# Performance work log

Hardware: AMD Instinct MI355X
Metric: run time of the kernel (lower is better)

Reference implementation:

```python
import jax, jax.numpy as jnp
import numpy as np

B, C, H, W = 32, 512, 32, 32
N_WORDS, WORD_DIM = 77, 256
HW2 = H * W


def setup_inputs() -> dict:
    key = jax.random.key(0)
    k1, k2, k3 = jax.random.split(key, 3)
    feat = jax.random.normal(k1, (B, C, H, W), dtype=jnp.float32)
    word_emb = jax.random.normal(k2, (B, N_WORDS, WORD_DIM), dtype=jnp.float32)
    # nn.Linear(word_dim, img_hw*img_hw): weight (out,in), bias (out,)
    W_fc = jax.random.normal(k3, (HW2, WORD_DIM), dtype=jnp.float32) * (1.0 / np.sqrt(WORD_DIM))
    b_fc = jnp.zeros((HW2,), dtype=jnp.float32)
    return {"feat": feat, "word_emb": word_emb, "W_fc": W_fc, "b_fc": b_fc}


def reference(feat, word_emb, W_fc, b_fc):
    b, c, h, w = feat.shape
    f = feat.reshape(b, c, h * w)                                   # (b, c, hw2)
    we = jnp.einsum('bnd,kd->bnk', word_emb, W_fc) + b_fc           # (b, n, hw2)
    we = jnp.swapaxes(we, 1, 2)                                     # (b, hw2, n)
    scores = jnp.einsum('bck,bkn->bcn', f, we)                      # (b, c, n)
    att = jax.nn.softmax(scores, axis=-1)                           # (b, c, n)
    att_feat = jnp.einsum('bcn,bkn->bck', att, we)                  # (b, c, hw2)
    return att_feat.reshape(b, c, h, w)
```

## Files before the change

### kernel.cpp

```cpp
#include <hip/hip_runtime.h>

#define B_    32
#define C_    512
#define HW2_  1024
#define NW    77
#define NP    80
#define NPT   96
#define WD    256

typedef unsigned int   uint32;
typedef unsigned short u16;
typedef __attribute__((ext_vector_type(8))) short bf16x8;
typedef __attribute__((ext_vector_type(4))) float f32x4;

#define MFMA(a, b, c) __builtin_amdgcn_mfma_f32_16x16x32_bf16(a, b, c, 0, 0, 0)

#define WE_ELN   ((size_t)B_ * 16 * NP * 8)
#define WET_ELN  ((size_t)B_ * HW2_ * 12)
#define W_ELN    ((size_t)HW2_ * 32)
#define E_ELN    ((size_t)B_ * NP * 32)

__device__ __forceinline__ void split1(float x, u16 &h, u16 &l) {
    uint32 u = __float_as_uint(x);
    h = (u16)(u >> 16);
    float r = x - __uint_as_float(u & 0xffff0000u);
    uint32 v = __float_as_uint(r);
    l = (u16)((v + 0x7fffu + ((v >> 16) & 1u)) >> 16);
}

__device__ __forceinline__ void split8(float4 a, float4 b, bf16x8 &h, bf16x8 &l) {
    float v[8] = {a.x, a.y, a.z, a.w, b.x, b.y, b.z, b.w};
    #pragma unroll
    for (int i = 0; i < 8; ++i) {
        u16 hh, ll; split1(v[i], hh, ll);
        h[i] = (short)hh; l[i] = (short)ll;
    }
}

__global__ __launch_bounds__(256) void split_pre(
    const float* __restrict__ W_fc, const float* __restrict__ word_emb,
    bf16x8* __restrict__ Wh, bf16x8* __restrict__ Wl,
    bf16x8* __restrict__ Eh, bf16x8* __restrict__ El)
{
    const int g = blockIdx.x * 256 + threadIdx.x;
    if (g < (int)W_ELN) {
        float4 x = *(const float4*)(W_fc + g * 8);
        float4 y = *(const float4*)(W_fc + g * 8 + 4);
        bf16x8 h, l; split8(x, y, h, l);
        Wh[g] = h; Wl[g] = l;
    } else {
        const int e = g - (int)W_ELN;
        const int b = e / 2560, r = e % 2560;
        const int n = r >> 5, gg = r & 31;
        bf16x8 h = (bf16x8)(short)0, l = h;
        if (n < NW) {
            const float* p = word_emb + ((size_t)(b * NW + n)) * WD + gg * 8;
            float4 x = *(const float4*)p, y = *(const float4*)(p + 4);
            split8(x, y, h, l);
        }
        Eh[e] = h; El[e] = l;
    }
}

__global__ __launch_bounds__(256) void we_gemm(
    const bf16x8* __restrict__ Wh, const bf16x8* __restrict__ Wl,
    const bf16x8* __restrict__ Eh, const bf16x8* __restrict__ El,
    const float* __restrict__ b_fc,
    bf16x8* __restrict__ we_hi, bf16x8* __restrict__ we_lo,
    bf16x8* __restrict__ weT_hi, bf16x8* __restrict__ weT_lo)
{
    __shared__ __align__(16) uint32 HL[NP][68];

    const int id = blockIdx.x;
    const int b  = (id & 7) + 8 * (id >> 7);
    const int q  = (id >> 3) & 15;
    const int kb = q * 64;
    const int t  = threadIdx.x;
    const int w  = t >> 6, lane = t & 63, lr = lane & 15, lg = lane >> 4;
    const int kout = kb + 16 * w + lr;

    f32x4 acc[5];
    #pragma unroll
    for (int m = 0; m < 5; ++m) acc[m] = (f32x4)0.0f;

    const bf16x8* wrh = Wh + kout * 32;
    const bf16x8* wrl = Wl + kout * 32;
    const bf16x8* ebh = Eh + (b * NP + lr) * 32;
    const bf16x8* ebl = El + (b * NP + lr) * 32;

    #pragma unroll
    for (int ks = 0; ks < 8; ++ks) {
        const int o = ks * 4 + lg;
        const bf16x8 bh = wrh[o], bl = wrl[o];
        #pragma unroll
        for (int m = 0; m < 5; ++m) {
            const bf16x8 ah = ebh[m * 512 + o];
            const bf16x8 al = ebl[m * 512 + o];
            acc[m] = MFMA(ah, bh, acc[m]);
            acc[m] = MFMA(ah, bl, acc[m]);
            acc[m] = MFMA(al, bh, acc[m]);
            acc[m] = MFMA(al, bl, acc[m]);
        }
    }

    const float bias = b_fc[kout];
    #pragma unroll
    for (int m = 0; m < 5; ++m)
        #pragma unroll
        for (int r = 0; r < 4; ++r) {
            u16 hh, ll; split1(acc[m][r] + bias, hh, ll);
            HL[16 * m + 4 * lg + r][16 * w + lr] = ((uint32)hh << 16) | ll;
        }
    __syncthreads();

    #pragma unroll
    for (int u0 = 0; u0 < 640; u0 += 256) {
        const int u = u0 + t;
        if (u < 640) {
            const int n = u >> 3, c8 = (u & 7) * 8;
            uint4 p0 = *(const uint4*)&HL[n][c8];
            uint4 p1 = *(const uint4*)&HL[n][c8 + 4];
            const uint32 pw[8] = {p0.x, p0.y, p0.z, p0.w, p1.x, p1.y, p1.z, p1.w};
            bf16x8 hv, lv;
            #pragma unroll
            for (int i = 0; i < 8; ++i) {
                hv[i] = (short)(pw[i] >> 16);
                lv[i] = (short)(pw[i] & 0xffffu);
            }
            const int o = ((b * 16 + q) * NP + n) * 8 + (u & 7);
            we_hi[o] = hv; we_lo[o] = lv;
        }
    }
    #pragma unroll
    for (int v0 = 0; v0 < 1536; v0 += 256) {
        const int v = v0 + t;
        const int sel = v >= 768;
        const int r2  = sel ? v - 768 : v;
        const int row = r2 / 12, g = r2 % 12;
        bf16x8 val;
        #pragma unroll
        for (int i = 0; i < 8; ++i) {
            const int n = g * 8 + i;
            const uint32 p = (n < NP) ? HL[n][row] : 0u;
            val[i] = (short)(sel ? (p & 0xffffu) : (p >> 16));
        }
        (sel ? weT_lo : weT_hi)[(b * HW2_ + kb + row) * 12 + g] = val;
    }
}

__global__ __launch_bounds__(256, 2) void attn_mfma(
    const float* __restrict__ feat,
    const bf16x8* __restrict__ we_hi, const bf16x8* __restrict__ we_lo,
    const bf16x8* __restrict__ weT_hi, const bf16x8* __restrict__ weT_lo,
    float* __restrict__ out)
{
    __shared__ __align__(16) float S[4][16][84];
    __shared__ __align__(16) u16   Ph[32][NPT];
    __shared__ __align__(16) u16   Pl[32][NPT];

    const int id  = blockIdx.x;
    const int b   = (id & 7) + 8 * (id >> 7);
    const int c0  = ((id >> 3) & 15) * 32;

    const int t    = threadIdx.x;
    const int h    = t >> 6;
    const int lane = t & 63, lr = lane & 15, lg = lane >> 4;

    f32x4 acc[2][5];
    #pragma unroll
    for (int s = 0; s < 2; ++s)
        #pragma unroll
        for (int m = 0; m < 5; ++m) acc[s][m] = (f32x4)0.0f;

    const float* frow0 = feat + (size_t)(b * C_ + c0 + lr) * HW2_;
    const float* frow1 = frow0 + 16 * HW2_;

    #pragma unroll
    for (int ks = 0; ks < 8; ++ks) {
        const int kk = h * 256 + ks * 32 + 8 * lg;
        bf16x8 fh0, fl0, fh1, fl1;
        {   float4 x = *(const float4*)(frow0 + kk);
            float4 y = *(const float4*)(frow0 + kk + 4);
            split8(x, y, fh0, fl0); }
        {   float4 x = *(const float4*)(frow1 + kk);
            float4 y = *(const float4*)(frow1 + kk + 4);
            split8(x, y, fh1, fl1); }
        const int qb  = (b * 16 + h * 4 + (ks >> 1)) * NP;
        const int sub = (ks & 1) * 4 + lg;
        #pragma unroll
        for (int m = 0; m < 5; ++m) {
            const int o = (qb + 16 * m + lr) * 8 + sub;
            const bf16x8 ah = we_hi[o];
            const bf16x8 al = we_lo[o];
            acc[0][m] = MFMA(ah, fh0, acc[0][m]);
            acc[0][m] = MFMA(ah, fl0, acc[0][m]);
            acc[0][m] = MFMA(al, fh0, acc[0][m]);
            acc[1][m] = MFMA(ah, fh1, acc[1][m]);
            acc[1][m] = MFMA(ah, fl1, acc[1][m]);
            acc[1][m] = MFMA(al, fh1, acc[1][m]);
        }
    }

    #pragma unroll
    for (int s = 0; s < 2; ++s) {
        #pragma unroll
        for (int m = 0; m < 5; ++m)
            #pragma unroll
            for (int r = 0; r < 4; ++r)
                S[h][lr][16 * m + 4 * lg + r] = acc[s][m][r];
        __syncthreads();
        {
            const int srow = 4 * h + (lane >> 4), scol = lane & 15;
            float v5[6];
            float mx = -3.0e38f;
            #pragma unroll
            for (int j = 0; j < 6; ++j) {
                const int n = scol + 16 * j;
                float sv = 0.f;
                if (j < 5) {
                    sv = S[0][srow][n] + S[1][srow][n] + S[2][srow][n] + S[3][srow][n];
                    if (n < NW) mx = fmaxf(mx, sv);
                }
                v5[j] = sv;
            }
            mx = fmaxf(mx, __shfl_xor(mx, 1));
            mx = fmaxf(mx, __shfl_xor(mx, 2));
            mx = fmaxf(mx, __shfl_xor(mx, 4));
            mx = fmaxf(mx, __shfl_xor(mx, 8));
            float sum = 0.f;
            #pragma unroll
            for (int j = 0; j < 6; ++j) {
                const int n = scol + 16 * j;
                const float e = (n < NW) ? __expf(v5[j] - mx) : 0.f;
                v5[j] = e; sum += e;
            }
            sum += __shfl_xor(sum, 1);
            sum += __shfl_xor(sum, 2);
            sum += __shfl_xor(sum, 4);
            sum += __shfl_xor(sum, 8);
            const float inv = 1.0f / sum;
            #pragma unroll
            for (int j = 0; j < 6; ++j) {
                const int n = scol + 16 * j;
                u16 ph, pl; split1(v5[j] * inv, ph, pl);
                Ph[16 * s + srow][n] = ph; Pl[16 * s + srow][n] = pl;
            }
        }
        __syncthreads();
    }

    bf16x8 pbh[2][3], pbl[2][3];
    #pragma unroll
    for (int s = 0; s < 2; ++s)
        #pragma unroll
        for (int ksn = 0; ksn < 3; ++ksn) {
            pbh[s][ksn] = *(const bf16x8*)&Ph[16 * s + lr][32 * ksn + 8 * lg];
            pbl[s][ksn] = *(const bf16x8*)&Pl[16 * s + lr][32 * ksn + 8 * lg];
        }
    const bf16x8* th = weT_hi + (size_t)b * HW2_ * 12;
    const bf16x8* tl = weT_lo + (size_t)b * HW2_ * 12;
    float* orow0 = out + (size_t)(b * C_ + c0 + lr) * HW2_;
    float* orow1 = orow0 + 16 * HW2_;

    #pragma unroll
    for (int tt = 0; tt < 16; ++tt) {
        const int row = h * 256 + tt * 16 + lr;
        bf16x8 wa[3], wb[3];
        #pragma unroll
        for (int ksn = 0; ksn < 3; ++ksn) {
            wa[ksn] = th[row * 12 + 4 * ksn + lg];
            wb[ksn] = tl[row * 12 + 4 * ksn + lg];
        }
        f32x4 o0 = (f32x4)0.0f, o1 = (f32x4)0.0f;
        #pragma unroll
        for (int ksn = 0; ksn < 3; ++ksn) {
            o0 = MFMA(wa[ksn], pbh[0][ksn], o0);
            o0 = MFMA(wa[ksn], pbl[0][ksn], o0);
            o0 = MFMA(wb[ksn], pbh[0][ksn], o0);
            o1 = MFMA(wa[ksn], pbh[1][ksn], o1);
            o1 = MFMA(wa[ksn], pbl[1][ksn], o1);
            o1 = MFMA(wb[ksn], pbh[1][ksn], o1);
        }
        const int col = h * 256 + tt * 16 + 4 * lg;
        *(float4*)(orow0 + col) = make_float4(o0[0], o0[1], o0[2], o0[3]);
        *(float4*)(orow1 + col) = make_float4(o1[0], o1[1], o1[2], o1[3]);
    }
}

extern "C" void kernel_launch(void* const* d_in, const int* in_sizes, int n_in,
                              void* d_out, int out_size, void* d_ws, size_t ws_size,
                              hipStream_t stream) {
    (void)in_sizes; (void)n_in; (void)out_size; (void)ws_size;
    const float* feat     = (const float*)d_in[0];
    const float* word_emb = (const float*)d_in[1];
    const float* W_fc     = (const float*)d_in[2];
    const float* b_fc     = (const float*)d_in[3];

    bf16x8* we_hi  = (bf16x8*)d_ws;
    bf16x8* we_lo  = we_hi  + WE_ELN;
    bf16x8* weT_hi = we_lo  + WE_ELN;
    bf16x8* weT_lo = weT_hi + WET_ELN;
    bf16x8* Wh     = weT_lo + WET_ELN;
    bf16x8* Wl     = Wh + W_ELN;
    bf16x8* Eh     = Wl + W_ELN;
    bf16x8* El     = Eh + E_ELN;

    split_pre<<<448, 256, 0, stream>>>(W_fc, word_emb, Wh, Wl, Eh, El);
    we_gemm<<<512, 256, 0, stream>>>(Wh, Wl, Eh, El, b_fc, we_hi, we_lo, weT_hi, weT_lo);
    attn_mfma<<<512, 256, 0, stream>>>(feat, we_hi, we_lo, weT_hi, weT_lo, (float*)d_out);
}
```

Baseline: 182.1 us.

## Fuse bf16 split prepass into we_gemm and prefetch feat loads in attention

Removes the split_pre kernel and has we_gemm read fp32 W_fc and word_emb directly, splitting them into hi/lo bf16 in registers. This drops one launch and a round trip of the split intermediates through global memory. The attention kernel now issues all feat loads up front, behind a sched_barrier, before converting and running the MFMAs, so load latency overlaps better. The cost is higher register pressure in both kernels, and word_emb is re-split redundantly by every block that reads it.

Result: no change. 184.3 us (+1.2%).

```diff
diff --git a/kernel.cpp b/kernel.cpp
--- a/kernel.cpp
+++ b/kernel.cpp
@@ -17,8 +17,6 @@
 
 #define WE_ELN   ((size_t)B_ * 16 * NP * 8)
 #define WET_ELN  ((size_t)B_ * HW2_ * 12)
-#define W_ELN    ((size_t)HW2_ * 32)
-#define E_ELN    ((size_t)B_ * NP * 32)
 
 __device__ __forceinline__ void split1(float x, u16 &h, u16 &l) {
     uint32 u = __float_as_uint(x);
@@ -37,34 +35,8 @@
     }
 }
 
-__global__ __launch_bounds__(256) void split_pre(
-    const float* __restrict__ W_fc, const float* __restrict__ word_emb,
-    bf16x8* __restrict__ Wh, bf16x8* __restrict__ Wl,
-    bf16x8* __restrict__ Eh, bf16x8* __restrict__ El)
-{
-    const int g = blockIdx.x * 256 + threadIdx.x;
-    if (g < (int)W_ELN) {
-        float4 x = *(const float4*)(W_fc + g * 8);
-        float4 y = *(const float4*)(W_fc + g * 8 + 4);
-        bf16x8 h, l; split8(x, y, h, l);
-        Wh[g] = h; Wl[g] = l;
-    } else {
-        const int e = g - (int)W_ELN;
-        const int b = e / 2560, r = e % 2560;
-        const int n = r >> 5, gg = r & 31;
-        bf16x8 h = (bf16x8)(short)0, l = h;
-        if (n < NW) {
-            const float* p = word_emb + ((size_t)(b * NW + n)) * WD + gg * 8;
-            float4 x = *(const float4*)p, y = *(const float4*)(p + 4);
-            split8(x, y, h, l);
-        }
-        Eh[e] = h; El[e] = l;
-    }
-}
-
-__global__ __launch_bounds__(256) void we_gemm(
-    const bf16x8* __restrict__ Wh, const bf16x8* __restrict__ Wl,
-    const bf16x8* __restrict__ Eh, const bf16x8* __restrict__ El,
+__global__ __launch_bounds__(256, 2) void we_gemm(
+    const float* __restrict__ word_emb, const float* __restrict__ W_fc,
     const float* __restrict__ b_fc,
     bf16x8* __restrict__ we_hi, bf16x8* __restrict__ we_lo,
     bf16x8* __restrict__ weT_hi, bf16x8* __restrict__ weT_lo)
@@ -79,27 +51,46 @@
     const int w  = t >> 6, lane = t & 63, lr = lane & 15, lg = lane >> 4;
     const int kout = kb + 16 * w + lr;
 
+    const float* wrow = W_fc + kout * WD;
+    float4 wx[8], wy[8];
+    #pragma unroll
+    for (int ks = 0; ks < 8; ++ks) {
+        const int dk = ks * 32 + 8 * lg;
+        wx[ks] = *(const float4*)(wrow + dk);
+        wy[ks] = *(const float4*)(wrow + dk + 4);
+    }
+    __builtin_amdgcn_sched_barrier(0);
+
+    bf16x8 bh[8], bl[8];
+    #pragma unroll
+    for (int ks = 0; ks < 8; ++ks) split8(wx[ks], wy[ks], bh[ks], bl[ks]);
+
     f32x4 acc[5];
     #pragma unroll
     for (int m = 0; m < 5; ++m) acc[m] = (f32x4)0.0f;
 
-    const bf16x8* wrh = Wh + kout * 32;
-    const bf16x8* wrl = Wl + kout * 32;
-    const bf16x8* ebh = Eh + (b * NP + lr) * 32;
-    const bf16x8* ebl = El + (b * NP + lr) * 32;
+    const float* emb = word_emb + b * NW * WD;
 
     #pragma unroll
     for (int ks = 0; ks < 8; ++ks) {
-        const int o = ks * 4 + lg;
-        const bf16x8 bh = wrh[o], bl = wrl[o];
+        const int dk = ks * 32 + 8 * lg;
+        bf16x8 ah[5], al[5];
         #pragma unroll
         for (int m = 0; m < 5; ++m) {
-            const bf16x8 ah = ebh[m * 512 + o];
-            const bf16x8 al = ebl[m * 512 + o];
-            acc[m] = MFMA(ah, bh, acc[m]);
-            acc[m] = MFMA(ah, bl, acc[m]);
-            acc[m] = MFMA(al, bh, acc[m]);
-            acc[m] = MFMA(al, bl, acc[m]);
+            const int n = 16 * m + lr;
+            float4 x = make_float4(0.f, 0.f, 0.f, 0.f), y = x;
+            if (n < NW) {
+                const float* p = emb + n * WD + dk;
+                x = *(const float4*)p; y = *(const float4*)(p + 4);
+            }
+            split8(x, y, ah[m], al[m]);
+        }
+        #pragma unroll
+        for (int m = 0; m < 5; ++m) {
+            acc[m] = MFMA(ah[m], bh[ks], acc[m]);
+            acc[m] = MFMA(ah[m], bl[ks], acc[m]);
+            acc[m] = MFMA(al[m], bh[ks], acc[m]);
+            acc[m] = MFMA(al[m], bl[ks], acc[m]);
         }
     }
 
@@ -166,25 +157,31 @@
     const int h    = t >> 6;
     const int lane = t & 63, lr = lane & 15, lg = lane >> 4;
 
-    f32x4 acc[2][5];
-    #pragma unroll
-    for (int s = 0; s < 2; ++s)
-        #pragma unroll
-        for (int m = 0; m < 5; ++m) acc[s][m] = (f32x4)0.0f;
-
     const float* frow0 = feat + (size_t)(b * C_ + c0 + lr) * HW2_;
     const float* frow1 = frow0 + 16 * HW2_;
 
+    float4 f0x[8], f0y[8], f1x[8], f1y[8];
     #pragma unroll
     for (int ks = 0; ks < 8; ++ks) {
         const int kk = h * 256 + ks * 32 + 8 * lg;
+        f0x[ks] = *(const float4*)(frow0 + kk);
+        f0y[ks] = *(const float4*)(frow0 + kk + 4);
+        f1x[ks] = *(const float4*)(frow1 + kk);
+        f1y[ks] = *(const float4*)(frow1 + kk + 4);
+    }
+    __builtin_amdgcn_sched_barrier(0);
+
+    f32x4 acc[2][5];
+    #pragma unroll
+    for (int s = 0; s < 2; ++s)
+        #pragma unroll
+        for (int m = 0; m < 5; ++m) acc[s][m] = (f32x4)0.0f;
+
+    #pragma unroll
+    for (int ks = 0; ks < 8; ++ks) {
         bf16x8 fh0, fl0, fh1, fl1;
-        {   float4 x = *(const float4*)(frow0 + kk);
-            float4 y = *(const float4*)(frow0 + kk + 4);
-            split8(x, y, fh0, fl0); }
-        {   float4 x = *(const float4*)(frow1 + kk);
-            float4 y = *(const float4*)(frow1 + kk + 4);
-            split8(x, y, fh1, fl1); }
+        split8(f0x[ks], f0y[ks], fh0, fl0);
+        split8(f1x[ks], f1y[ks], fh1, fl1);
         const int qb  = (b * 16 + h * 4 + (ks >> 1)) * NP;
         const int sub = (ks & 1) * 4 + lg;
         #pragma unroll
@@ -300,12 +297,7 @@
     bf16x8* we_lo  = we_hi  + WE_ELN;
     bf16x8* weT_hi = we_lo  + WE_ELN;
     bf16x8* weT_lo = weT_hi + WET_ELN;
-    bf16x8* Wh     = weT_lo + WET_ELN;
-    bf16x8* Wl     = Wh + W_ELN;
-    bf16x8* Eh     = Wl + W_ELN;
-    bf16x8* El     = Eh + E_ELN;
-
-    split_pre<<<448, 256, 0, stream>>>(W_fc, word_emb, Wh, Wl, Eh, El);
-    we_gemm<<<512, 256, 0, stream>>>(Wh, Wl, Eh, El, b_fc, we_hi, we_lo, weT_hi, weT_lo);
+
+    we_gemm<<<512, 256, 0, stream>>>(word_emb, W_fc, b_fc, we_hi, we_lo, weT_hi, weT_lo);
     attn_mfma<<<512, 256, 0, stream>>>(feat, we_hi, we_lo, weT_hi, weT_lo, (float*)d_out);
 }
```
